# Kernel optimization log

Measured on AMD Instinct MI355X. Metric: run time of the kernel, lower is better.

## Reference

```python
import jax, jax.numpy as jnp
import numpy as np

E = 262144  # num edges
H = 8       # num heads
N = 2048    # num nodes


def setup_inputs() -> dict:
    key = jax.random.key(0)
    k1, k2, k3 = jax.random.split(key, 3)
    edge_index = jax.random.randint(k1, (2, E), 0, N, dtype=jnp.int64)
    edge_score = jax.random.uniform(k2, (E,), dtype=jnp.float32)
    # nn.Linear(3, H): weight [H, 3], bias [H] (kaiming-uniform-ish init scale)
    bound = 1.0 / np.sqrt(3.0)
    kw, kb = jax.random.split(k3)
    W = jax.random.uniform(kw, (H, 3), minval=-bound, maxval=bound, dtype=jnp.float32)
    b = jax.random.uniform(kb, (H,), minval=-bound, maxval=bound, dtype=jnp.float32)
    return {"edge_index": edge_index, "edge_score": edge_score, "W": W, "b": b, "num_nodes": N}


def reference(edge_index, edge_score, W, b, num_nodes):
    row, col = edge_index[0], edge_index[1]
    # edge features: [E, 3] = (row, col, score)
    features = jnp.stack([row.astype(jnp.float32), col.astype(jnp.float32), edge_score], axis=-1)
    # tiny GEMM + sigmoid: [E, H]
    bias_per_edge = jax.nn.sigmoid(features @ W.T + b)
    # scatter into dense (H, N, N) bias; starts at zero so set == original
    # torch's `buf[h,row,col] = buf[h,row,col] + v` (non-accumulating assign on zeros)
    edge_bias = jnp.zeros((W.shape[0], num_nodes, num_nodes), dtype=bias_per_edge.dtype)
    edge_bias = edge_bias.at[:, row, col].set(bias_per_edge.T)
    return edge_bias
```

## Files before the change

kernel.cpp:

```cpp
#include <hip/hip_runtime.h>

#define NNODES 2048
#define NHEADS 8
#define NN (NNODES * NNODES)

__global__ __launch_bounds__(256) void winner_kernel(const int* __restrict__ ei, int E,
                                                     int* __restrict__ winner) {
    int e = blockIdx.x * blockDim.x + threadIdx.x;
    if (e >= E) return;
    int row = ei[e];
    int col = ei[E + e];
    atomicMax(&winner[row * NNODES + col], e);
}

__global__ __launch_bounds__(256) void write_kernel(const int* __restrict__ winner,
                                                    const float* __restrict__ edge_score,
                                                    const float* __restrict__ W,
                                                    const float* __restrict__ b,
                                                    float* __restrict__ out) {
    int t = blockIdx.x * blockDim.x + threadIdx.x;
    int cell0 = t << 2;
    if (cell0 >= NN) return;

    const int4 w4 = *reinterpret_cast<const int4*>(winner + cell0);
    const int wi[4] = {w4.x, w4.y, w4.z, w4.w};

    const float row  = (float)(cell0 >> 11);
    const float colb = (float)(cell0 & (NNODES - 1));

    float sc[4];
#pragma unroll
    for (int i = 0; i < 4; ++i) sc[i] = (wi[i] >= 0) ? edge_score[wi[i]] : 0.0f;

#pragma unroll
    for (int h = 0; h < NHEADS; ++h) {
        const float W0 = W[h * 3 + 0];
        const float W1 = W[h * 3 + 1];
        const float W2 = W[h * 3 + 2];
        const float B  = b[h];
        float4 v;
        float* vp = reinterpret_cast<float*>(&v);
#pragma unroll
        for (int i = 0; i < 4; ++i) {
            const float x = fmaf(row, W0, fmaf(colb + (float)i, W1, fmaf(sc[i], W2, B)));
            const float s = 1.0f / (1.0f + __expf(-x));
            vp[i] = (wi[i] >= 0) ? s : 0.0f;
        }
        *reinterpret_cast<float4*>(out + (size_t)h * NN + cell0) = v;
    }
}

extern "C" void kernel_launch(void* const* d_in, const int* in_sizes, int n_in,
                              void* d_out, int out_size, void* d_ws, size_t ws_size,
                              hipStream_t stream) {
    const int*   edge_index = (const int*)d_in[0];
    const float* edge_score = (const float*)d_in[1];
    const float* W          = (const float*)d_in[2];
    const float* b          = (const float*)d_in[3];
    float*       out        = (float*)d_out;
    const int E = in_sizes[1];

    int* winner = (int*)d_ws;

    hipMemsetAsync(winner, 0xFF, (size_t)NN * sizeof(int), stream);

    winner_kernel<<<(E + 255) / 256, 256, 0, stream>>>(edge_index, E, winner);

    write_kernel<<<NN / (4 * 256), 256, 0, stream>>>(winner, edge_score, W, b, out);
}
```

Before: 47.74 us.

## Replace dense per-cell write pass with zero-fill memset plus sparse edge scatter

The dense kernel that computed every output cell from the winner table is replaced. The output is now zero-filled with a memset, and a second edge-parallel kernel has each winning edge compute its eight sigmoid values and write them to its own cell. The aim is to cut sigmoid work and winner-table reads down to the edges that actually exist. In exchange it adds a full-size memset of the output and millions of scattered 4-byte writes spread across eight head planes, which may use bandwidth poorly.

```diff
diff --git a/kernel.cpp b/kernel.cpp
--- a/kernel.cpp
+++ b/kernel.cpp
@@ -4,49 +4,40 @@
 #define NHEADS 8
 #define NN (NNODES * NNODES)
 
-__global__ __launch_bounds__(256) void winner_kernel(const int* __restrict__ ei, int E,
-                                                     int* __restrict__ winner) {
+#define WINNER_BYTES ((size_t)NN * sizeof(int))
+
+__global__ __launch_bounds__(256) void edge_max_kernel(const int* __restrict__ ei,
+                                                       int E,
+                                                       int* __restrict__ winner) {
     int e = blockIdx.x * blockDim.x + threadIdx.x;
     if (e >= E) return;
-    int row = ei[e];
-    int col = ei[E + e];
+    const int row = ei[e];
+    const int col = ei[E + e];
     atomicMax(&winner[row * NNODES + col], e);
 }
 
-__global__ __launch_bounds__(256) void write_kernel(const int* __restrict__ winner,
-                                                    const float* __restrict__ edge_score,
-                                                    const float* __restrict__ W,
-                                                    const float* __restrict__ b,
-                                                    float* __restrict__ out) {
-    int t = blockIdx.x * blockDim.x + threadIdx.x;
-    int cell0 = t << 2;
-    if (cell0 >= NN) return;
+__global__ __launch_bounds__(256) void scatter_kernel(const int* __restrict__ ei,
+                                                      const float* __restrict__ edge_score,
+                                                      const float* __restrict__ W,
+                                                      const float* __restrict__ b,
+                                                      int E,
+                                                      const int* __restrict__ winner,
+                                                      float* __restrict__ out) {
+    int e = blockIdx.x * blockDim.x + threadIdx.x;
+    if (e >= E) return;
+    const int row = ei[e];
+    const int col = ei[E + e];
+    const int cell = row * NNODES + col;
+    if (winner[cell] != e) return;
 
-    const int4 w4 = *reinterpret_cast<const int4*>(winner + cell0);
-    const int wi[4] = {w4.x, w4.y, w4.z, w4.w};
-
-    const float row  = (float)(cell0 >> 11);
-    const float colb = (float)(cell0 & (NNODES - 1));
-
-    float sc[4];
-#pragma unroll
-    for (int i = 0; i < 4; ++i) sc[i] = (wi[i] >= 0) ? edge_score[wi[i]] : 0.0f;
-
+    const float fr = (float)row, fc = (float)col, sc = edge_score[e];
 #pragma unroll
     for (int h = 0; h < NHEADS; ++h) {
-        const float W0 = W[h * 3 + 0];
-        const float W1 = W[h * 3 + 1];
-        const float W2 = W[h * 3 + 2];
-        const float B  = b[h];
-        float4 v;
-        float* vp = reinterpret_cast<float*>(&v);
-#pragma unroll
-        for (int i = 0; i < 4; ++i) {
-            const float x = fmaf(row, W0, fmaf(colb + (float)i, W1, fmaf(sc[i], W2, B)));
-            const float s = 1.0f / (1.0f + __expf(-x));
-            vp[i] = (wi[i] >= 0) ? s : 0.0f;
-        }
-        *reinterpret_cast<float4*>(out + (size_t)h * NN + cell0) = v;
+        const float x = fmaf(fr, W[3 * h + 0],
+                        fmaf(fc, W[3 * h + 1],
+                        fmaf(sc, W[3 * h + 2], b[h])));
+        const float s = 1.0f / (1.0f + __expf(-x));
+        out[(size_t)h * NN + cell] = s;
     }
 }
 
@@ -62,9 +53,11 @@
 
     int* winner = (int*)d_ws;
 
-    hipMemsetAsync(winner, 0xFF, (size_t)NN * sizeof(int), stream);
+    hipMemsetAsync(winner, 0xFF, WINNER_BYTES, stream);
+    hipMemsetAsync(out, 0, (size_t)out_size * sizeof(float), stream);
 
-    winner_kernel<<<(E + 255) / 256, 256, 0, stream>>>(edge_index, E, winner);
-
-    write_kernel<<<NN / (4 * 256), 256, 0, stream>>>(winner, edge_score, W, b, out);
+    const int blocks = (E + 255) / 256;
+    edge_max_kernel<<<blocks, 256, 0, stream>>>(edge_index, E, winner);
+    scatter_kernel<<<blocks, 256, 0, stream>>>(edge_index, edge_score, W, b,
+                                               E, winner, out);
 }
```

New measurement: 76.64 us. 60.6% more time.
